# Performance work log

Measured on AMD Instinct MI355X. Metric: run time of the kernel, lower is better.

Reference implementation:

```python
import jax, jax.numpy as jnp
import numpy as np

# RBF_Conv2d config (matches init_kwargs)
KH = KW = 3
STRIDE = 1
OUT_CH = 256
IN_CH = 64
STD = 2.0  # gauss RBF std (activate_param[0])


def setup_inputs() -> dict:
    key = jax.random.key(0)
    k1, k2 = jax.random.split(key)
    x = jax.random.normal(k1, (16, IN_CH, 56, 56), dtype=jnp.float32)
    # kaiming_uniform_ on fan_in = IN_CH*KH*KW = 576 -> bound = sqrt(6/576)
    bound = float(np.sqrt(6.0 / (IN_CH * KH * KW)))
    weight = jax.random.uniform(k2, (OUT_CH, IN_CH * KH * KW), dtype=jnp.float32,
                                minval=-bound, maxval=bound)
    return {"x": x, "weight": weight}


def _cdist_conv(x, weight):
    # im2col: [B, C*KH*KW, Ho, Wo]; channel ordering (c, kh, kw) matches F.unfold
    patches = jax.lax.conv_general_dilated_patches(
        x, (KH, KW), (STRIDE, STRIDE), 'VALID')
    B, Kdim, Ho, Wo = patches.shape
    win = patches.reshape(B, Kdim, Ho * Wo).transpose(0, 2, 1)  # [B, P, K]
    # Euclidean distance via the expansion ||w||^2 + ||c||^2 - 2 w.c (no [B,P,K,O] tensor)
    w2 = jnp.sum(win * win, axis=-1, keepdims=True)            # [B, P, 1]
    c2 = jnp.sum(weight * weight, axis=-1)[None, None, :]      # [1, 1, O]
    d2 = w2 + c2 - 2.0 * jnp.einsum('bpk,ok->bpo', win, weight)
    dist = jnp.sqrt(jnp.maximum(d2, 1e-12))                    # [B, P, O]
    return dist, (B, Ho, Wo)


def reference(x, weight):
    dist, (B, Ho, Wo) = _cdist_conv(x, weight)
    # gauss RBF: exp(-d^2 / (2*std^2))
    act = jnp.exp(-(dist * dist) / (2.0 * STD * STD))
    # permute back to [B, O, Ho, Wo] like the torch code
    return act.transpose(0, 2, 1).reshape(B, OUT_CH, Ho, Wo)
```

## Files before the change

### kernel.cpp

```cpp
#include <hip/hip_runtime.h>
#include <hip/hip_bf16.h>
#include <stdint.h>

#define BATCH 16
#define IN_CH 64
#define HIN 56
#define WIN_ 56
#define HO 54
#define WO 54
#define P_PER_B (HO*WO)
#define P_PAD 2944
#define OUT_CH 256
#define KDIM 576
#define NPIX (HIN*WIN_)
#define XT_PIX 3264

typedef __attribute__((ext_vector_type(8))) short short8;
typedef __attribute__((ext_vector_type(4))) float f32x4;

__device__ __forceinline__ unsigned short f2bf(float f) {
    unsigned int u = __float_as_uint(f);
    unsigned int r = (u + 0x7fffu + ((u >> 16) & 1u)) >> 16;
    return (unsigned short)r;
}


__global__ void prep_weight(const float* __restrict__ w, short* __restrict__ wbf,
                            float* __restrict__ c2) {
    int o = blockIdx.x;
    int lane = threadIdx.x;
    float s = 0.f;
    #pragma unroll
    for (int j = 0; j < 9; ++j) {
        int k = j * 64 + lane;
        int c = k / 9, tap = k % 9;
        float v = w[o * KDIM + k];
        s += v * v;
        ((unsigned short*)wbf)[((size_t)tap * OUT_CH + o) * 64 + c] = f2bf(v);
    }
    #pragma unroll
    for (int off = 32; off > 0; off >>= 1) s += __shfl_down(s, off);
    if (lane == 0) c2[o] = s;
}

__global__ __launch_bounds__(256) void transpose_kernel(
    const float* __restrict__ x, short* __restrict__ xT, float* __restrict__ s) {
    __shared__ short lds[64 * 65];
    __shared__ float red[256];
    const int b    = blockIdx.x / 49;
    const int pix0 = (blockIdx.x % 49) * 64;
    const int tid  = threadIdx.x;
    const int quarter = tid >> 6;
    const int pix  = tid & 63;
    const float* xb = x + (size_t)b * IN_CH * NPIX + pix0 + pix;
    float acc = 0.f;
    #pragma unroll
    for (int it = 0; it < 16; ++it) {
        int c = quarter * 16 + it;
        float v = xb[c * NPIX];
        acc += v * v;
        lds[pix * 65 + c] = (short)f2bf(v);
    }
    red[tid] = acc;
    __syncthreads();
    const int cs = tid & 63;
    short* xTb = xT + ((size_t)b * XT_PIX + pix0) * 64;
    #pragma unroll
    for (int it = 0; it < 16; ++it) {
        int pixs = quarter * 16 + it;
        xTb[(size_t)pixs * 64 + cs] = lds[pixs * 65 + cs];
    }
    if (tid < 64)
        s[b * NPIX + pix0 + tid] = red[tid] + red[64 + tid] + red[128 + tid] + red[192 + tid];
}

__global__ void w2_kernel(const float* __restrict__ s, float* __restrict__ w2) {
    int t = blockIdx.x * 256 + threadIdx.x;
    if (t >= BATCH * P_PER_B) return;
    int b = t / P_PER_B, p = t % P_PER_B;
    int oh = p / WO, ow = p % WO;
    const float* sp = s + b * NPIX + oh * WIN_ + ow;
    float acc = 0.f;
    #pragma unroll
    for (int kh = 0; kh < 3; ++kh)
        #pragma unroll
        for (int kw = 0; kw < 3; ++kw)
            acc += sp[kh * WIN_ + kw];
    w2[b * P_PAD + p] = acc;
}


#define AS1(p) ((const __attribute__((address_space(1))) void*)(p))
#define AS3(p) ((__attribute__((address_space(3))) void*)(p))

__global__ __launch_bounds__(512, 4) void gemm_rbf(
    const short* __restrict__ xT, const short* __restrict__ wbf,
    const float* __restrict__ w2, const float* __restrict__ c2,
    float* __restrict__ out) {
    __shared__ __align__(16) short lds_a[352 * 64];
    __shared__ __align__(16) short lds_b[2 * 128 * 64];

    const int mt = blockIdx.x;
    const int b  = mt / 23;
    const int p0 = (mt % 23) * 128;
    const int n0 = blockIdx.y * 128;

    const int tid  = threadIdx.x;
    const int wave = tid >> 6;
    const int lane = tid & 63;
    const int r16  = lane & 15;
    const int quad = lane >> 4;
    const int wm = (wave >> 2) * 64;
    const int wn = (wave & 3) * 32;

    const int oh_base  = p0 / WO;
    const int ihw_base = oh_base * WIN_;

    const int srow = lane >> 3;
    const int scx  = (lane & 7) ^ srow;

    const short* aSrc = xT + ((size_t)b * XT_PIX + ihw_base + srow) * 64 + scx * 8;
    #pragma unroll
    for (int i = 0; i < 6; ++i) {
        int rb8 = (wave * 6 + i) * 8;
        if (rb8 < 352)
            __builtin_amdgcn_global_load_lds(AS1(aSrc + (size_t)rb8 * 64),
                                             AS3(lds_a + rb8 * 64), 16, 0, 0);
    }
    const short* gbB = wbf + ((size_t)n0 + wave * 16 + srow) * 64 + scx * 8;
    #pragma unroll
    for (int i = 0; i < 2; ++i)
        __builtin_amdgcn_global_load_lds(AS1(gbB + (size_t)i * 8 * 64),
                                         AS3(lds_b + (wave * 2 + i) * 512), 16, 0, 0);

    int ihw_rel[4];
    #pragma unroll
    for (int ms = 0; ms < 4; ++ms) {
        int p = p0 + wm + ms * 16 + r16;
        if (p > P_PER_B - 1) p = P_PER_B - 1;
        int oh = p / WO, ow = p - oh * WO;
        ihw_rel[ms] = oh * WIN_ + ow - ihw_base;
    }
    const int xq = r16 & 7;

    f32x4 acc[4][2];
    #pragma unroll
    for (int i = 0; i < 4; ++i)
        #pragma unroll
        for (int j = 0; j < 2; ++j)
            acc[i][j] = (f32x4){0.f, 0.f, 0.f, 0.f};

    constexpr int dtab_l[9] = {0, 1, 2, 56, 57, 58, 112, 113, 114};
    #pragma unroll
    for (int kt = 0; kt < 9; ++kt) {
        asm volatile("s_waitcnt vmcnt(0)" ::: "memory");
        __builtin_amdgcn_s_barrier();
        __builtin_amdgcn_sched_barrier(0);
        if (kt < 8) {
            short* dstB = lds_b + ((kt + 1) & 1) * (128 * 64);
            #pragma unroll
            for (int i = 0; i < 2; ++i)
                __builtin_amdgcn_global_load_lds(
                    AS1(gbB + ((size_t)(kt + 1) * OUT_CH + i * 8) * 64),
                    AS3(dstB + (wave * 2 + i) * 512), 16, 0, 0);
        }
        const short* lb = lds_b + (kt & 1) * (128 * 64);
        const int dt = dtab_l[kt];
        __builtin_amdgcn_s_setprio(1);
        #pragma unroll
        for (int ks = 0; ks < 2; ++ks) {
            short8 af[4], bfr[2];
            #pragma unroll
            for (int ms = 0; ms < 4; ++ms) {
                int rl = ihw_rel[ms] + dt;
                af[ms] = *(const short8*)(lds_a + rl * 64
                                                + (((ks * 4 + quad) ^ (rl & 7)) * 8));
            }
            #pragma unroll
            for (int ns = 0; ns < 2; ++ns)
                bfr[ns] = *(const short8*)(lb + (wn + ns * 16 + r16) * 64
                                              + (((ks * 4 + quad) ^ xq) * 8));
            #pragma unroll
            for (int ms = 0; ms < 4; ++ms)
                #pragma unroll
                for (int ns = 0; ns < 2; ++ns)
                    acc[ms][ns] = __builtin_amdgcn_mfma_f32_16x16x32_bf16(
                        af[ms], bfr[ns], acc[ms][ns], 0, 0, 0);
        }
        __builtin_amdgcn_s_setprio(0);
    }

    float* lf = (float*)lds_a;
    const int col  = tid & 31;
    const int rowb = tid >> 5;
    const int pcol = p0 + col * 4;
    const bool pok = (pcol < P_PER_B);
    f32x4 w2v = *(const f32x4*)(w2 + b * P_PAD + pcol);
    const int myChunk = (wave >> 1) & 1;

    #pragma unroll
    for (int s = 0; s < 2; ++s) {
        __syncthreads();
        if (myChunk == s) {
            #pragma unroll
            for (int ms = 0; ms < 4; ++ms) {
                int pl = wm + ms * 16 + quad * 4;
                #pragma unroll
                for (int ns = 0; ns < 2; ++ns) {
                    int od = (wave & 1) * 32 + ns * 16 + r16;
                    *(f32x4*)(lf + od * 132 + pl) = acc[ms][ns];
                }
            }
        }
        __syncthreads();
        #pragma unroll
        for (int pass = 0; pass < 4; ++pass) {
            int row = pass * 16 + rowb;
            int o   = n0 + s * 64 + row;
            f32x4 a = *(const f32x4*)(lf + row * 132 + col * 4);
            float c2o = c2[o];
            f32x4 v;
            #pragma unroll
            for (int r = 0; r < 4; ++r) {
                float d2 = w2v[r] + c2o - 2.0f * a[r];
                d2 = fmaxf(d2, 1e-12f);
                v[r] = __expf(-0.125f * d2);
            }
            if (pok)
                *(f32x4*)(out + ((size_t)(b * OUT_CH + o)) * P_PER_B + pcol) = v;
        }
    }
}


extern "C" void kernel_launch(void* const* d_in, const int* in_sizes, int n_in,
                              void* d_out, int out_size, void* d_ws, size_t ws_size,
                              hipStream_t stream) {
    const float* x = (const float*)d_in[0];
    const float* w = (const float*)d_in[1];
    float* out = (float*)d_out;

    char* ws = (char*)d_ws;
    const size_t wbf_bytes = (size_t)OUT_CH * KDIM * 2;
    const size_t c2_bytes  = 1024;
    const size_t w2_bytes  = (size_t)BATCH * P_PAD * 4;
    const size_t s_bytes   = (size_t)BATCH * NPIX * 4;
    short* wbf = (short*)ws;
    float* c2  = (float*)(ws + wbf_bytes);
    float* w2  = (float*)(ws + wbf_bytes + c2_bytes);
    float* s   = (float*)(ws + wbf_bytes + c2_bytes + w2_bytes);
    short* xT  = (short*)(ws + wbf_bytes + c2_bytes + w2_bytes + s_bytes);

    hipLaunchKernelGGL(prep_weight, dim3(OUT_CH), dim3(64), 0, stream, w, wbf, c2);
    hipLaunchKernelGGL(transpose_kernel, dim3(16 * 49), dim3(256), 0, stream, x, xT, s);
    hipLaunchKernelGGL(w2_kernel, dim3((BATCH * P_PER_B + 255) / 256), dim3(256), 0, stream, s, w2);
    hipLaunchKernelGGL(gemm_rbf, dim3(23 * BATCH, OUT_CH / 128), dim3(512), 0, stream,
                       xT, wbf, w2, c2, out);
}
```

Measured before the change: 104.7 us.

## Process both output-channel halves per block, reusing the A tile in LDS

Each GEMM block now loops over both 128-channel halves of the output instead of launching a second grid dimension, so the im2col A tile in LDS is loaded once and reused for all 256 channels. The first half's epilogue goes through the spare B buffer in small 16-row chunks while the second half's first B tile is prefetched, overlapping the loads with the epilogue. Block indices are also remapped across the 368 blocks, presumably to spread them over XCDs. This halves block count and A traffic but serialises twice the work per block and adds many barriers, which may lower parallelism.

```diff
diff --git a/kernel.cpp b/kernel.cpp
--- a/kernel.cpp
+++ b/kernel.cpp
@@ -100,10 +100,10 @@
     __shared__ __align__(16) short lds_a[352 * 64];
     __shared__ __align__(16) short lds_b[2 * 128 * 64];
 
-    const int mt = blockIdx.x;
-    const int b  = mt / 23;
-    const int p0 = (mt % 23) * 128;
-    const int n0 = blockIdx.y * 128;
+    const int bid = blockIdx.x;
+    const int mt  = (bid & 7) * 46 + (bid >> 3);
+    const int b   = mt / 23;
+    const int p0  = (mt % 23) * 128;
 
     const int tid  = threadIdx.x;
     const int wave = tid >> 6;
@@ -127,10 +127,11 @@
             __builtin_amdgcn_global_load_lds(AS1(aSrc + (size_t)rb8 * 64),
                                              AS3(lds_a + rb8 * 64), 16, 0, 0);
     }
-    const short* gbB = wbf + ((size_t)n0 + wave * 16 + srow) * 64 + scx * 8;
+    const short* gbB0 = wbf + ((size_t)(wave * 16 + srow)) * 64 + scx * 8;
+    const short* gbB1 = gbB0 + (size_t)128 * 64;
     #pragma unroll
     for (int i = 0; i < 2; ++i)
-        __builtin_amdgcn_global_load_lds(AS1(gbB + (size_t)i * 8 * 64),
+        __builtin_amdgcn_global_load_lds(AS1(gbB0 + (size_t)i * 8 * 64),
                                          AS3(lds_b + (wave * 2 + i) * 512), 16, 0, 0);
 
     int ihw_rel[4];
@@ -143,91 +144,142 @@
     }
     const int xq = r16 & 7;
 
-    f32x4 acc[4][2];
-    #pragma unroll
-    for (int i = 0; i < 4; ++i)
+    const int ecol = tid & 31;
+    const int erow = tid >> 5;
+    const int pcol = p0 + ecol * 4;
+    const bool pok = (pcol < P_PER_B);
+    f32x4 w2v = *(const f32x4*)(w2 + b * P_PAD + pcol);
+
+    __syncthreads();
+
+    constexpr int dtab_l[9] = {0, 1, 2, 56, 57, 58, 112, 113, 114};
+    #pragma unroll
+    for (int nt = 0; nt < 2; ++nt) {
+        const short* gB = (nt == 0) ? gbB0 : gbB1;
+
+        f32x4 acc[4][2];
         #pragma unroll
-        for (int j = 0; j < 2; ++j)
-            acc[i][j] = (f32x4){0.f, 0.f, 0.f, 0.f};
-
-    constexpr int dtab_l[9] = {0, 1, 2, 56, 57, 58, 112, 113, 114};
-    #pragma unroll
-    for (int kt = 0; kt < 9; ++kt) {
-        asm volatile("s_waitcnt vmcnt(0)" ::: "memory");
+        for (int i = 0; i < 4; ++i)
+            #pragma unroll
+            for (int j = 0; j < 2; ++j)
+                acc[i][j] = (f32x4){0.f, 0.f, 0.f, 0.f};
+
+        #pragma unroll
+        for (int kt = 0; kt < 9; ++kt) {
+            if (nt == 1 && kt == 0)
+                asm volatile("s_waitcnt vmcnt(8)" ::: "memory");
+            else
+                asm volatile("s_waitcnt vmcnt(0)" ::: "memory");
+            __builtin_amdgcn_s_barrier();
+            __builtin_amdgcn_sched_barrier(0);
+            if (kt < 8) {
+                short* dstB = lds_b + ((kt + 1) & 1) * (128 * 64);
+                #pragma unroll
+                for (int i = 0; i < 2; ++i)
+                    __builtin_amdgcn_global_load_lds(
+                        AS1(gB + ((size_t)(kt + 1) * OUT_CH + i * 8) * 64),
+                        AS3(dstB + (wave * 2 + i) * 512), 16, 0, 0);
+            }
+            const short* lb = lds_b + (kt & 1) * (128 * 64);
+            const int dt = dtab_l[kt];
+            __builtin_amdgcn_s_setprio(1);
+            #pragma unroll
+            for (int ks = 0; ks < 2; ++ks) {
+                short8 af[4], bfr[2];
+                #pragma unroll
+                for (int ms = 0; ms < 4; ++ms) {
+                    int rl = ihw_rel[ms] + dt;
+                    af[ms] = *(const short8*)(lds_a + rl * 64
+                                                    + (((ks * 4 + quad) ^ (rl & 7)) * 8));
+                }
+                #pragma unroll
+                for (int ns = 0; ns < 2; ++ns)
+                    bfr[ns] = *(const short8*)(lb + (wn + ns * 16 + r16) * 64
+                                                  + (((ks * 4 + quad) ^ xq) * 8));
+                #pragma unroll
+                for (int ms = 0; ms < 4; ++ms)
+                    #pragma unroll
+                    for (int ns = 0; ns < 2; ++ns)
+                        acc[ms][ns] = __builtin_amdgcn_mfma_f32_16x16x32_bf16(
+                            af[ms], bfr[ns], acc[ms][ns], 0, 0, 0);
+            }
+            __builtin_amdgcn_s_setprio(0);
+        }
+
         __builtin_amdgcn_s_barrier();
         __builtin_amdgcn_sched_barrier(0);
-        if (kt < 8) {
-            short* dstB = lds_b + ((kt + 1) & 1) * (128 * 64);
+
+        if (nt == 0) {
             #pragma unroll
             for (int i = 0; i < 2; ++i)
-                __builtin_amdgcn_global_load_lds(
-                    AS1(gbB + ((size_t)(kt + 1) * OUT_CH + i * 8) * 64),
-                    AS3(dstB + (wave * 2 + i) * 512), 16, 0, 0);
-        }
-        const short* lb = lds_b + (kt & 1) * (128 * 64);
-        const int dt = dtab_l[kt];
-        __builtin_amdgcn_s_setprio(1);
-        #pragma unroll
-        for (int ks = 0; ks < 2; ++ks) {
-            short8 af[4], bfr[2];
-            #pragma unroll
-            for (int ms = 0; ms < 4; ++ms) {
-                int rl = ihw_rel[ms] + dt;
-                af[ms] = *(const short8*)(lds_a + rl * 64
-                                                + (((ks * 4 + quad) ^ (rl & 7)) * 8));
+                __builtin_amdgcn_global_load_lds(AS1(gbB1 + (size_t)i * 8 * 64),
+                                                 AS3(lds_b + (wave * 2 + i) * 512), 16, 0, 0);
+            float* lf = (float*)(lds_b + 128 * 64);
+            #pragma unroll
+            for (int c = 0; c < 8; ++c) {
+                if ((wave & 3) == (c >> 1)) {
+                    const int ns = c & 1;
+                    #pragma unroll
+                    for (int ms = 0; ms < 4; ++ms)
+                        *(f32x4*)(lf + r16 * 132 + wm + ms * 16 + quad * 4) = acc[ms][ns];
+                }
+                asm volatile("s_waitcnt lgkmcnt(0)" ::: "memory");
+                __builtin_amdgcn_s_barrier();
+                __builtin_amdgcn_sched_barrier(0);
+                {
+                    int o = c * 16 + erow;
+                    f32x4 a = *(const f32x4*)(lf + erow * 132 + ecol * 4);
+                    float c2o = c2[o];
+                    f32x4 v;
+                    #pragma unroll
+                    for (int r = 0; r < 4; ++r) {
+                        float d2 = w2v[r] + c2o - 2.0f * a[r];
+                        d2 = fmaxf(d2, 1e-12f);
+                        v[r] = __expf(-0.125f * d2);
+                    }
+                    if (pok)
+                        *(f32x4*)(out + ((size_t)(b * OUT_CH + o)) * P_PER_B + pcol) = v;
+                }
+                __builtin_amdgcn_s_barrier();
+                __builtin_amdgcn_sched_barrier(0);
             }
-            #pragma unroll
-            for (int ns = 0; ns < 2; ++ns)
-                bfr[ns] = *(const short8*)(lb + (wn + ns * 16 + r16) * 64
-                                              + (((ks * 4 + quad) ^ xq) * 8));
-            #pragma unroll
-            for (int ms = 0; ms < 4; ++ms)
-                #pragma unroll
-                for (int ns = 0; ns < 2; ++ns)
-                    acc[ms][ns] = __builtin_amdgcn_mfma_f32_16x16x32_bf16(
-                        af[ms], bfr[ns], acc[ms][ns], 0, 0, 0);
-        }
-        __builtin_amdgcn_s_setprio(0);
-    }
-
-    float* lf = (float*)lds_a;
-    const int col  = tid & 31;
-    const int rowb = tid >> 5;
-    const int pcol = p0 + col * 4;
-    const bool pok = (pcol < P_PER_B);
-    f32x4 w2v = *(const f32x4*)(w2 + b * P_PAD + pcol);
-    const int myChunk = (wave >> 1) & 1;
-
-    #pragma unroll
-    for (int s = 0; s < 2; ++s) {
-        __syncthreads();
-        if (myChunk == s) {
-            #pragma unroll
-            for (int ms = 0; ms < 4; ++ms) {
-                int pl = wm + ms * 16 + quad * 4;
-                #pragma unroll
-                for (int ns = 0; ns < 2; ++ns) {
-                    int od = (wave & 1) * 32 + ns * 16 + r16;
-                    *(f32x4*)(lf + od * 132 + pl) = acc[ms][ns];
-                }
+        } else {
+            float* lf = (float*)lds_a;
+            #pragma unroll
+            for (int s = 0; s < 2; ++s) {
+                if (((wave >> 1) & 1) == s) {
+                    #pragma unroll
+                    for (int ms = 0; ms < 4; ++ms) {
+                        int pl = wm + ms * 16 + quad * 4;
+                        #pragma unroll
+                        for (int ns = 0; ns < 2; ++ns) {
+                            int od = (wave & 1) * 32 + ns * 16 + r16;
+                            *(f32x4*)(lf + od * 132 + pl) = acc[ms][ns];
+                        }
+                    }
+                }
+                asm volatile("s_waitcnt lgkmcnt(0)" ::: "memory");
+                __builtin_amdgcn_s_barrier();
+                __builtin_amdgcn_sched_barrier(0);
+                #pragma unroll
+                for (int pass = 0; pass < 4; ++pass) {
+                    int row = pass * 16 + erow;
+                    int o   = 128 + s * 64 + row;
+                    f32x4 a = *(const f32x4*)(lf + row * 132 + ecol * 4);
+                    float c2o = c2[o];
+                    f32x4 v;
+                    #pragma unroll
+                    for (int r = 0; r < 4; ++r) {
+                        float d2 = w2v[r] + c2o - 2.0f * a[r];
+                        d2 = fmaxf(d2, 1e-12f);
+                        v[r] = __expf(-0.125f * d2);
+                    }
+                    if (pok)
+                        *(f32x4*)(out + ((size_t)(b * OUT_CH + o)) * P_PER_B + pcol) = v;
+                }
+                __builtin_amdgcn_s_barrier();
+                __builtin_amdgcn_sched_barrier(0);
             }
-        }
-        __syncthreads();
-        #pragma unroll
-        for (int pass = 0; pass < 4; ++pass) {
-            int row = pass * 16 + rowb;
-            int o   = n0 + s * 64 + row;
-            f32x4 a = *(const f32x4*)(lf + row * 132 + col * 4);
-            float c2o = c2[o];
-            f32x4 v;
-            #pragma unroll
-            for (int r = 0; r < 4; ++r) {
-                float d2 = w2v[r] + c2o - 2.0f * a[r];
-                d2 = fmaxf(d2, 1e-12f);
-                v[r] = __expf(-0.125f * d2);
-            }
-            if (pok)
-                *(f32x4*)(out + ((size_t)(b * OUT_CH + o)) * P_PER_B + pcol) = v;
         }
     }
 }
@@ -254,6 +306,6 @@
     hipLaunchKernelGGL(prep_weight, dim3(OUT_CH), dim3(64), 0, stream, w, wbf, c2);
     hipLaunchKernelGGL(transpose_kernel, dim3(16 * 49), dim3(256), 0, stream, x, xT, s);
     hipLaunchKernelGGL(w2_kernel, dim3((BATCH * P_PER_B + 255) / 256), dim3(256), 0, stream, s, w2);
-    hipLaunchKernelGGL(gemm_rbf, dim3(23 * BATCH, OUT_CH / 128), dim3(512), 0, stream,
+    hipLaunchKernelGGL(gemm_rbf, dim3(368), dim3(512), 0, stream,
                        xT, wbf, w2, c2, out);
 }
```

Measured after the change: 112.8 us. 1.08x slower.

## Fuse w2 window-sum into GEMM prologue and vectorize transpose loads

Applied to the files above, without the earlier changes.

Removes the separate w2_kernel launch and its intermediate buffer: the GEMM now computes each pixel's 3x3 window sum of per-pixel squared norms directly from the s array before the main loop. The transpose kernel is changed to read x with float4 vector loads, with the channel reduction regrouped in LDS. This saves one kernel launch and a round trip through global memory. In exchange, each GEMM block redoes 36 scattered loads per thread, and this work is repeated across both N blocks.

```diff
diff --git a/kernel.cpp b/kernel.cpp
--- a/kernel.cpp
+++ b/kernel.cpp
@@ -46,47 +46,41 @@
 __global__ __launch_bounds__(256) void transpose_kernel(
     const float* __restrict__ x, short* __restrict__ xT, float* __restrict__ s) {
     __shared__ short lds[64 * 65];
-    __shared__ float red[256];
+    __shared__ float red4[256 * 4];
     const int b    = blockIdx.x / 49;
     const int pix0 = (blockIdx.x % 49) * 64;
     const int tid  = threadIdx.x;
-    const int quarter = tid >> 6;
-    const int pix  = tid & 63;
-    const float* xb = x + (size_t)b * IN_CH * NPIX + pix0 + pix;
-    float acc = 0.f;
-    #pragma unroll
-    for (int it = 0; it < 16; ++it) {
-        int c = quarter * 16 + it;
-        float v = xb[c * NPIX];
-        acc += v * v;
-        lds[pix * 65 + c] = (short)f2bf(v);
-    }
-    red[tid] = acc;
+    const int cq = tid >> 4;
+    const int pg = tid & 15;
+    const float* xb = x + (size_t)b * IN_CH * NPIX + pix0 + pg * 4;
+    f32x4 accp = (f32x4){0.f, 0.f, 0.f, 0.f};
+    #pragma unroll
+    for (int it = 0; it < 4; ++it) {
+        int c = it * 16 + cq;
+        f32x4 v = *(const f32x4*)(xb + (size_t)c * NPIX);
+        #pragma unroll
+        for (int j = 0; j < 4; ++j) {
+            accp[j] += v[j] * v[j];
+            lds[(pg * 4 + j) * 65 + c] = (short)f2bf(v[j]);
+        }
+    }
+    *(f32x4*)(red4 + tid * 4) = accp;
     __syncthreads();
     const int cs = tid & 63;
+    const int quarter = tid >> 6;
     short* xTb = xT + ((size_t)b * XT_PIX + pix0) * 64;
     #pragma unroll
     for (int it = 0; it < 16; ++it) {
         int pixs = quarter * 16 + it;
         xTb[(size_t)pixs * 64 + cs] = lds[pixs * 65 + cs];
     }
-    if (tid < 64)
-        s[b * NPIX + pix0 + tid] = red[tid] + red[64 + tid] + red[128 + tid] + red[192 + tid];
-}
-
-__global__ void w2_kernel(const float* __restrict__ s, float* __restrict__ w2) {
-    int t = blockIdx.x * 256 + threadIdx.x;
-    if (t >= BATCH * P_PER_B) return;
-    int b = t / P_PER_B, p = t % P_PER_B;
-    int oh = p / WO, ow = p % WO;
-    const float* sp = s + b * NPIX + oh * WIN_ + ow;
-    float acc = 0.f;
-    #pragma unroll
-    for (int kh = 0; kh < 3; ++kh)
-        #pragma unroll
-        for (int kw = 0; kw < 3; ++kw)
-            acc += sp[kh * WIN_ + kw];
-    w2[b * P_PAD + p] = acc;
+    if (tid < 64) {
+        float sacc = 0.f;
+        #pragma unroll
+        for (int c16 = 0; c16 < 16; ++c16)
+            sacc += red4[(c16 * 16 + (tid >> 2)) * 4 + (tid & 3)];
+        s[b * NPIX + pix0 + tid] = sacc;
+    }
 }
 
 
@@ -95,7 +89,7 @@
 
 __global__ __launch_bounds__(512, 4) void gemm_rbf(
     const short* __restrict__ xT, const short* __restrict__ wbf,
-    const float* __restrict__ w2, const float* __restrict__ c2,
+    const float* __restrict__ s, const float* __restrict__ c2,
     float* __restrict__ out) {
     __shared__ __align__(16) short lds_a[352 * 64];
     __shared__ __align__(16) short lds_b[2 * 128 * 64];
@@ -143,6 +137,29 @@
     }
     const int xq = r16 & 7;
 
+    const int ecol = tid & 31;
+    const int erow = tid >> 5;
+    const int pcol = p0 + ecol * 4;
+    const bool pok = (pcol < P_PER_B);
+    f32x4 w2v;
+    {
+        const int pbase = pok ? pcol : (P_PER_B - 4);
+        const float* sb = s + b * NPIX;
+        #pragma unroll
+        for (int r = 0; r < 4; ++r) {
+            int p = pbase + r;
+            int oh = p / WO, ow = p - oh * WO;
+            const float* sp = sb + oh * WIN_ + ow;
+            float a0 = 0.f;
+            #pragma unroll
+            for (int kh = 0; kh < 3; ++kh)
+                #pragma unroll
+                for (int kw = 0; kw < 3; ++kw)
+                    a0 += sp[kh * WIN_ + kw];
+            w2v[r] = a0;
+        }
+    }
+
     f32x4 acc[4][2];
     #pragma unroll
     for (int i = 0; i < 4; ++i)
@@ -191,17 +208,12 @@
     }
 
     float* lf = (float*)lds_a;
-    const int col  = tid & 31;
-    const int rowb = tid >> 5;
-    const int pcol = p0 + col * 4;
-    const bool pok = (pcol < P_PER_B);
-    f32x4 w2v = *(const f32x4*)(w2 + b * P_PAD + pcol);
     const int myChunk = (wave >> 1) & 1;
 
     #pragma unroll
-    for (int s = 0; s < 2; ++s) {
+    for (int sc = 0; sc < 2; ++sc) {
         __syncthreads();
-        if (myChunk == s) {
+        if (myChunk == sc) {
             #pragma unroll
             for (int ms = 0; ms < 4; ++ms) {
                 int pl = wm + ms * 16 + quad * 4;
@@ -215,9 +227,9 @@
         __syncthreads();
         #pragma unroll
         for (int pass = 0; pass < 4; ++pass) {
-            int row = pass * 16 + rowb;
-            int o   = n0 + s * 64 + row;
-            f32x4 a = *(const f32x4*)(lf + row * 132 + col * 4);
+            int row = pass * 16 + erow;
+            int o   = n0 + sc * 64 + row;
+            f32x4 a = *(const f32x4*)(lf + row * 132 + ecol * 4);
             float c2o = c2[o];
             f32x4 v;
             #pragma unroll
@@ -243,17 +255,14 @@
     char* ws = (char*)d_ws;
     const size_t wbf_bytes = (size_t)OUT_CH * KDIM * 2;
     const size_t c2_bytes  = 1024;
-    const size_t w2_bytes  = (size_t)BATCH * P_PAD * 4;
     const size_t s_bytes   = (size_t)BATCH * NPIX * 4;
     short* wbf = (short*)ws;
     float* c2  = (float*)(ws + wbf_bytes);
-    float* w2  = (float*)(ws + wbf_bytes + c2_bytes);
-    float* s   = (float*)(ws + wbf_bytes + c2_bytes + w2_bytes);
-    short* xT  = (short*)(ws + wbf_bytes + c2_bytes + w2_bytes + s_bytes);
+    float* s   = (float*)(ws + wbf_bytes + c2_bytes);
+    short* xT  = (short*)(ws + wbf_bytes + c2_bytes + s_bytes);
 
     hipLaunchKernelGGL(prep_weight, dim3(OUT_CH), dim3(64), 0, stream, w, wbf, c2);
     hipLaunchKernelGGL(transpose_kernel, dim3(16 * 49), dim3(256), 0, stream, x, xT, s);
-    hipLaunchKernelGGL(w2_kernel, dim3((BATCH * P_PER_B + 255) / 256), dim3(256), 0, stream, s, w2);
     hipLaunchKernelGGL(gemm_rbf, dim3(23 * BATCH, OUT_CH / 128), dim3(512), 0, stream,
-                       xT, wbf, w2, c2, out);
-}
+                       xT, wbf, s, c2, out);
+}
```

After: 103.4 us. About the same (-1.3%).
